# Kernel tuning notes

Hardware: AMD Instinct MI355X
Metric: run time of the kernel (lower is better)

## Reference

```python
import jax, jax.numpy as jnp
import numpy as np

# ----- module constants (from init_kwargs) -----
N = 1024          # Np = [N, N]
NZ = 16           # number of slices (O.shape[3])
NA = 0.65         # objective NA
WL = 0.5          # wavelength (um)
PS = 6.5          # camera pixel size (um)
MAG = 20.0        # magnification
PS_EFF = PS / MAG
DZ = 10.0 * PS / MAG                 # slice spacing (code overwrites wl/na**2)
KAPPA = 2.0 * np.pi * DZ / WL        # imag part of self.k
K = np.complex64(1j * KAPPA)         # self.k as a complex scalar


def _grids():
    c = (np.arange(N) - N // 2) * PS_EFF
    xx, yy = np.meshgrid(c, c)                       # spatial grids
    f = (np.arange(N) - N // 2) / (PS_EFF * N)
    uxx, uyy = np.meshgrid(f, f)                     # frequency grids
    return xx, yy, uxx, uyy

_XX, _YY, _UXX, _UYY = _grids()
_URR = _UXX ** 2 + _UYY ** 2
_PC = (_URR < (NA / WL) ** 2).astype(np.float64)     # centered pupil


def _fresnel(dz):
    # genFrensel: band-limited angular-spectrum kernel, stored in fft order
    kz = np.sqrt(np.maximum(_PC * ((1.0 / WL) ** 2 - _URR), 0.0))
    kern = _PC * np.exp(1j * 2.0 * np.pi * dz * kz)
    return jnp.asarray(np.fft.fftshift(kern).astype(np.complex64))

PUPIL = jnp.asarray(np.fft.fftshift(_PC).astype(np.complex64))   # fft order
PROPKERN = _fresnel(DZ)
PROPKERN_FOCUS = _fresnel(-DZ * (NZ - 1) / 2.0)
XX = jnp.asarray(_XX, jnp.float32)
YY = jnp.asarray(_YY, jnp.float32)


def _prop(u, kern):
    # torch.fft / torch.ifft pair == unnormalized fft2 / normalized ifft2
    return jnp.fft.ifft2(jnp.fft.fft2(u) * kern)


def _plane_wave(na_illum):
    dfx = 1.0 / (PS_EFF * N)
    tilt = jnp.round((na_illum / WL) / dfx) * dfx    # snap tilt to freq grid
    phase = 2.0 * np.pi * (tilt[0] * XX + tilt[1] * YY)
    return jnp.exp(1j * phase)                        # complex64


def _ms_grad(O, intensity, na_illum):
    """Faithful translation of Multislice.grad. O: [N,N,NZ] complex64."""
    T = jnp.exp(K * O)                                # per-slice transmittance
    u = _plane_wave(na_illum)
    # forward multislice propagation
    for zz in range(NZ):
        u = T[..., zz] * u
        if zz < NZ - 1:
            u = _prop(u, PROPKERN)
    # refocus to stack center, apply pupil
    u_ref = _prop(u, PROPKERN_FOCUS)
    u_pup = _prop(u_ref, PUPIL)
    # amplitude-replacement residual
    abs_field = jnp.abs(u_pup)
    comp = jnp.sqrt(intensity) * u_pup / abs_field
    residual = u_pup - comp
    # back-propagate residual
    u_bp = _prop(residual, jnp.conj(PUPIL))
    u_bp = _prop(u_bp, jnp.conj(PROPKERN_FOCUS))
    # reverse slice loop accumulating per-slice gradient
    grads = [None] * NZ
    for zz in range(NZ - 1, -1, -1):
        grads[zz] = u_bp * jnp.conj(u) * jnp.conj(T[..., zz]) * np.conj(K)
        if zz > 0:
            u_bp = _prop(u_bp * jnp.conj(T[..., zz]), jnp.conj(PROPKERN))
            u = _prop(u, jnp.conj(PROPKERN))
            u = u / T[..., zz - 1]
    return jnp.stack(grads, axis=-1)                  # [N,N,NZ] complex


def setup_inputs() -> dict:
    key = jax.random.key(0)
    k1, k2, k3 = jax.random.split(key, 3)
    # small-valued object so exp(i*KAPPA*O) stays bounded (KAPPA ~ 40.8)
    x = jax.random.normal(k1, (N, N, 2, NZ), jnp.float32) * 0.01
    meas = jax.random.uniform(k2, (N, N), jnp.float32) + 0.1
    na_illum = jax.random.uniform(k3, (2,), jnp.float32) * 0.2
    alpha = jnp.full((1,), 0.01, jnp.float32)
    return {"x": x, "meas": meas, "na_illum": na_illum, "alpha": alpha}


def reference(x, meas, na_illum, alpha):
    # forward: x + step(x) = x - alpha * grad(x, meas, na_illum)
    O = x[..., 0, :] + 1j * x[..., 1, :]              # [N,N,NZ] complex64
    g = _ms_grad(O, meas, na_illum)
    out = O - alpha[0] * g
    return jnp.stack((out.real, out.imag), axis=2)    # back to [N,N,2,NZ]
```

## Files before the change

### kernel.cpp

```cpp
#include <hip/hip_runtime.h>
#include <math.h>


#define NN (1024*1024)
#define KAPPA 40.840704496667314f
#define TWO_PI_F 6.2831853071795865f
#define DFX_D 0.0030048076923076925
#define RRCUT 187177
#define F(i) ((i) + ((i)>>4))

#define JT 0
#define JT_WP 1
#define JN 2
#define JRESID 3

__device__ __forceinline__ float2 cmulf(float2 a, float2 b){
    return make_float2(a.x*b.x - a.y*b.y, a.x*b.y + a.y*b.x);
}
__device__ __forceinline__ float2 cmulcj(float2 a, float2 b){
    return make_float2(a.x*b.x + a.y*b.y, a.y*b.x - a.x*b.y);
}
__device__ __forceinline__ float2 f2add(float2 a, float2 b){ return make_float2(a.x+b.x, a.y+b.y); }
__device__ __forceinline__ float2 f2sub(float2 a, float2 b){ return make_float2(a.x-b.x, a.y-b.y); }

__device__ __forceinline__ void fill_tw(float2* tw, int tid){
    #pragma unroll
    for (int k = tid; k < 512; k += 256){
        float s, c; sincosf(-(float)k * (TWO_PI_F/1024.0f), &s, &c);
        tw[k] = make_float2(c, s);
    }
}

__device__ __forceinline__ void dif_ph1(float2 r[8], const float2* tw, int lane){
    float2 a, d;
    #pragma unroll
    for (int k=0;k<4;++k){
        a=r[k]; d=f2sub(r[k],r[k+4]);
        r[k]=f2add(a,r[k+4]);
        r[k+4]=cmulf(d, tw[lane+128*k]);
    }
    float2 w20 = tw[lane<<1], w21 = tw[(lane+128)<<1];
    a=r[0]; d=f2sub(r[0],r[2]); r[0]=f2add(a,r[2]); r[2]=cmulf(d,w20);
    a=r[1]; d=f2sub(r[1],r[3]); r[1]=f2add(a,r[3]); r[3]=cmulf(d,w21);
    a=r[4]; d=f2sub(r[4],r[6]); r[4]=f2add(a,r[6]); r[6]=cmulf(d,w20);
    a=r[5]; d=f2sub(r[5],r[7]); r[5]=f2add(a,r[7]); r[7]=cmulf(d,w21);
    float2 w3 = tw[lane<<2];
    a=r[0]; d=f2sub(r[0],r[1]); r[0]=f2add(a,r[1]); r[1]=cmulf(d,w3);
    a=r[2]; d=f2sub(r[2],r[3]); r[2]=f2add(a,r[3]); r[3]=cmulf(d,w3);
    a=r[4]; d=f2sub(r[4],r[5]); r[4]=f2add(a,r[5]); r[5]=cmulf(d,w3);
    a=r[6]; d=f2sub(r[6],r[7]); r[6]=f2add(a,r[7]); r[7]=cmulf(d,w3);
}
__device__ __forceinline__ void dit_ph1(float2 r[8], const float2* tw, int lane){
    float2 a, b;
    float2 w3 = tw[lane<<2];
    a=r[0]; b=cmulcj(r[1],w3); r[0]=f2add(a,b); r[1]=f2sub(a,b);
    a=r[2]; b=cmulcj(r[3],w3); r[2]=f2add(a,b); r[3]=f2sub(a,b);
    a=r[4]; b=cmulcj(r[5],w3); r[4]=f2add(a,b); r[5]=f2sub(a,b);
    a=r[6]; b=cmulcj(r[7],w3); r[6]=f2add(a,b); r[7]=f2sub(a,b);
    float2 w20 = tw[lane<<1], w21 = tw[(lane+128)<<1];
    a=r[0]; b=cmulcj(r[2],w20); r[0]=f2add(a,b); r[2]=f2sub(a,b);
    a=r[1]; b=cmulcj(r[3],w21); r[1]=f2add(a,b); r[3]=f2sub(a,b);
    a=r[4]; b=cmulcj(r[6],w20); r[4]=f2add(a,b); r[6]=f2sub(a,b);
    a=r[5]; b=cmulcj(r[7],w21); r[5]=f2add(a,b); r[7]=f2sub(a,b);
    #pragma unroll
    for (int k=0;k<4;++k){
        a=r[k]; b=cmulcj(r[k+4], tw[lane+128*k]);
        r[k]=f2add(a,b); r[k+4]=f2sub(a,b);
    }
}
__device__ __forceinline__ void dif_ph2(float2 r[8], const float2* tw, int m0){
    float2 a, d;
    #pragma unroll
    for (int k=0;k<4;++k){
        a=r[k]; d=f2sub(r[k],r[k+4]);
        r[k]=f2add(a,r[k+4]);
        r[k+4]=cmulf(d, tw[(m0+16*k)<<3]);
    }
    float2 w40 = tw[m0<<4], w41 = tw[(m0+16)<<4];
    a=r[0]; d=f2sub(r[0],r[2]); r[0]=f2add(a,r[2]); r[2]=cmulf(d,w40);
    a=r[1]; d=f2sub(r[1],r[3]); r[1]=f2add(a,r[3]); r[3]=cmulf(d,w41);
    a=r[4]; d=f2sub(r[4],r[6]); r[4]=f2add(a,r[6]); r[6]=cmulf(d,w40);
    a=r[5]; d=f2sub(r[5],r[7]); r[5]=f2add(a,r[7]); r[7]=cmulf(d,w41);
    float2 w5 = tw[m0<<5];
    a=r[0]; d=f2sub(r[0],r[1]); r[0]=f2add(a,r[1]); r[1]=cmulf(d,w5);
    a=r[2]; d=f2sub(r[2],r[3]); r[2]=f2add(a,r[3]); r[3]=cmulf(d,w5);
    a=r[4]; d=f2sub(r[4],r[5]); r[4]=f2add(a,r[5]); r[5]=cmulf(d,w5);
    a=r[6]; d=f2sub(r[6],r[7]); r[6]=f2add(a,r[7]); r[7]=cmulf(d,w5);
}
__device__ __forceinline__ void dit_ph2(float2 r[8], const float2* tw, int m0){
    float2 a, b;
    float2 w5 = tw[m0<<5];
    a=r[0]; b=cmulcj(r[1],w5); r[0]=f2add(a,b); r[1]=f2sub(a,b);
    a=r[2]; b=cmulcj(r[3],w5); r[2]=f2add(a,b); r[3]=f2sub(a,b);
    a=r[4]; b=cmulcj(r[5],w5); r[4]=f2add(a,b); r[5]=f2sub(a,b);
    a=r[6]; b=cmulcj(r[7],w5); r[6]=f2add(a,b); r[7]=f2sub(a,b);
    float2 w40 = tw[m0<<4], w41 = tw[(m0+16)<<4];
    a=r[0]; b=cmulcj(r[2],w40); r[0]=f2add(a,b); r[2]=f2sub(a,b);
    a=r[1]; b=cmulcj(r[3],w41); r[1]=f2add(a,b); r[3]=f2sub(a,b);
    a=r[4]; b=cmulcj(r[6],w40); r[4]=f2add(a,b); r[6]=f2sub(a,b);
    a=r[5]; b=cmulcj(r[7],w41); r[5]=f2add(a,b); r[7]=f2sub(a,b);
    #pragma unroll
    for (int k=0;k<4;++k){
        a=r[k]; b=cmulcj(r[k+4], tw[(m0+16*k)<<3]);
        r[k]=f2add(a,b); r[k+4]=f2sub(a,b);
    }
}
__device__ __forceinline__ void dif_reg(float2 r[8]){
    const float C = 0.70710678118654752f;
    float2 a,d;
    a=r[0]; d=f2sub(r[0],r[4]); r[0]=f2add(a,r[4]); r[4]=d;
    a=r[1]; d=f2sub(r[1],r[5]); r[1]=f2add(a,r[5]); r[5]=make_float2(C*(d.x+d.y), C*(d.y-d.x));
    a=r[2]; d=f2sub(r[2],r[6]); r[2]=f2add(a,r[6]); r[6]=make_float2(d.y, -d.x);
    a=r[3]; d=f2sub(r[3],r[7]); r[3]=f2add(a,r[7]); r[7]=make_float2(C*(d.y-d.x), -C*(d.x+d.y));
    a=r[0]; r[0]=f2add(a,r[2]); r[2]=f2sub(a,r[2]);
    a=r[1]; d=f2sub(r[1],r[3]); r[1]=f2add(a,r[3]); r[3]=make_float2(d.y,-d.x);
    a=r[4]; r[4]=f2add(a,r[6]); r[6]=f2sub(a,r[6]);
    a=r[5]; d=f2sub(r[5],r[7]); r[5]=f2add(a,r[7]); r[7]=make_float2(d.y,-d.x);
    a=r[0]; r[0]=f2add(a,r[1]); r[1]=f2sub(a,r[1]);
    a=r[2]; r[2]=f2add(a,r[3]); r[3]=f2sub(a,r[3]);
    a=r[4]; r[4]=f2add(a,r[5]); r[5]=f2sub(a,r[5]);
    a=r[6]; r[6]=f2add(a,r[7]); r[7]=f2sub(a,r[7]);
}
__device__ __forceinline__ void dit_reg(float2 r[8]){
    const float C = 0.70710678118654752f;
    float2 a,b,t;
    a=r[0]; r[0]=f2add(a,r[1]); r[1]=f2sub(a,r[1]);
    a=r[2]; r[2]=f2add(a,r[3]); r[3]=f2sub(a,r[3]);
    a=r[4]; r[4]=f2add(a,r[5]); r[5]=f2sub(a,r[5]);
    a=r[6]; r[6]=f2add(a,r[7]); r[7]=f2sub(a,r[7]);
    a=r[0]; r[0]=f2add(a,r[2]); r[2]=f2sub(a,r[2]);
    a=r[1]; t=r[3]; b=make_float2(-t.y, t.x); r[1]=f2add(a,b); r[3]=f2sub(a,b);
    a=r[4]; r[4]=f2add(a,r[6]); r[6]=f2sub(a,r[6]);
    a=r[5]; t=r[7]; b=make_float2(-t.y, t.x); r[5]=f2add(a,b); r[7]=f2sub(a,b);
    a=r[0]; r[0]=f2add(a,r[4]); r[4]=f2sub(a,r[4]);
    a=r[1]; t=r[5]; b=make_float2(C*(t.x-t.y), C*(t.x+t.y)); r[1]=f2add(a,b); r[5]=f2sub(a,b);
    a=r[2]; t=r[6]; b=make_float2(-t.y, t.x); r[2]=f2add(a,b); r[6]=f2sub(a,b);
    a=r[3]; t=r[7]; b=make_float2(-C*(t.x+t.y), C*(t.x-t.y)); r[3]=f2add(a,b); r[7]=f2sub(a,b);
}

__device__ __forceinline__ void st128l(float2* L, int ro, int lane, const float2 r[8]){
    #pragma unroll
    for (int k=0;k<8;++k) L[F(ro + lane + 128*k)] = r[k];
}
__device__ __forceinline__ void ld128l(const float2* L, int ro, int lane, float2 r[8]){
    #pragma unroll
    for (int k=0;k<8;++k) r[k] = L[F(ro + lane + 128*k)];
}
__device__ __forceinline__ void st16l(float2* L, int ro, int lane, const float2 r[8]){
    int b = lane>>4, m0 = lane&15, q = ro + 128*b + m0;
    #pragma unroll
    for (int k=0;k<8;++k) L[F(q + 16*k)] = r[k];
}
__device__ __forceinline__ void ld16l(const float2* L, int ro, int lane, float2 r[8]){
    int b = lane>>4, m0 = lane&15, q = ro + 128*b + m0;
    #pragma unroll
    for (int k=0;k<8;++k) r[k] = L[F(q + 16*k)];
}
__device__ __forceinline__ void st8l(float2* L, int ro, int lane, const float2 r[8]){
    int q = ro + 8*lane;
    #pragma unroll
    for (int i=0;i<8;++i) L[F(q + i)] = r[i];
}
__device__ __forceinline__ void ldfold_dif(const float2* L, int ro, int lane,
                                           const float2* tw, float2 r[8]){
    int rr = lane>>1, sub = lane&1, q = ro + 16*rr;
    #pragma unroll
    for (int i=0;i<8;++i){
        float2 x = L[F(q + i)];
        float2 y = L[F(q + 8 + i)];
        r[i] = sub ? cmulf(f2sub(x,y), tw[i<<6]) : f2add(x,y);
    }
}
__device__ __forceinline__ void ldfold_dit(const float2* L, int ro, int lane,
                                           const float2* tw, float2 r[8]){
    int b = lane>>4, m0 = lane&15, m0s = m0&7;
    float2 w = tw[m0s<<6];
    int q = ro + 128*b + m0s;
    #pragma unroll
    for (int k=0;k<8;++k){
        float2 x = L[F(q + 16*k)];
        float2 y = L[F(q + 16*k + 8)];
        float2 bb = cmulcj(y, w);
        r[k] = (m0 < 8) ? f2add(x,bb) : f2sub(x,bb);
    }
}
__device__ __forceinline__ void load8g(const float2* src, int lane, float2 r[8]){
    const float4* s4 = (const float4*)src + lane*4;
    #pragma unroll
    for (int m=0;m<4;++m){
        float4 v = s4[m];
        r[2*m]   = make_float2(v.x, v.y);
        r[2*m+1] = make_float2(v.z, v.w);
    }
}
__device__ __forceinline__ void twrite2(const float2* L, int tid, float2* dst,
                                        int r0, float s){
    #pragma unroll
    for (int k=0;k<4;++k){
        int c = tid + (k<<8);
        float2 a0 = L[F(c)], a1 = L[F(1024+c)];
        ((float4*)(dst + ((size_t)c<<10) + r0))[0] =
            make_float4(a0.x*s, a0.y*s, a1.x*s, a1.y*s);
    }
}

__global__ void __launch_bounds__(256) k_kern(float2* __restrict__ kp,
                                              float2* __restrict__ kf){
    int idx = blockIdx.x*256 + threadIdx.x;
    int j = idx >> 10, i = idx & 1023;
    int a = __brev((unsigned)i) >> 22;
    int b = __brev((unsigned)j) >> 22;
    int ra = a - (a >= 512 ? 1024 : 0);
    int rb = b - (b >= 512 ? 1024 : 0);
    int rr = ra*ra + rb*rb;
    float2 p = make_float2(0.f,0.f), f = make_float2(0.f,0.f);
    if (rr <= RRCUT){
        double urr = (double)rr * (DFX_D*DFX_D);
        double kz = sqrt(4.0 - urr);
        double s1,c1,s2,c2;
        sincos(6.283185307179586 * 3.25    * kz, &s1, &c1);
        sincos(6.283185307179586 * -24.375 * kz, &s2, &c2);
        p = make_float2((float)c1,(float)s1);
        f = make_float2((float)c2,(float)s2);
    }
    kp[idx] = p; kf[idx] = f;
}

__global__ void __launch_bounds__(256) k_T(const float4* __restrict__ x,
                                           float2* __restrict__ T){
    int idx = blockIdx.x*256 + threadIdx.x;
    int p = idx >> 2;
    int q = idx & 3;
    float4 vr = x[(size_t)p*8 + q];
    float4 vi = x[(size_t)p*8 + 4 + q];
    const float* fr = (const float*)&vr;
    const float* fi = (const float*)&vi;
    #pragma unroll
    for (int j=0;j<4;++j){
        int z = 4*q + j;
        float amp = __expf(-KAPPA*fi[j]);
        float s, c; __sincosf(KAPPA*fr[j], &s, &c);
        T[(size_t)z*NN + p] = make_float2(amp*c, amp*s);
    }
}

__global__ void __launch_bounds__(256) k_head(float2* __restrict__ dst,
                                              const float2* __restrict__ T0,
                                              const float* __restrict__ nail){
    __shared__ float2 A[2176], B[2176], tw[512];
    const int tid = threadIdx.x;
    fill_tw(tw, tid);
    const int row = tid>>7, lane = tid&127, ro = row<<10, m0 = lane&15;
    const int r0 = blockIdx.x*2;
    const size_t gbase = ((size_t)(r0+row))<<10;
    float dfx = (float)DFX_D;
    float t0 = rintf(nail[0]*2.0f/dfx)*dfx;
    float t1 = rintf(nail[1]*2.0f/dfx)*dfx;
    float yv = (float)((r0+row) - 512) * 0.325f;
    float2 r[8];
    #pragma unroll
    for (int k=0;k<8;++k){
        int col = lane + 128*k;
        float2 tv = T0[gbase + col];
        float xv = (float)(col - 512) * 0.325f;
        float s0, c0; sincosf(TWO_PI_F*(t0*xv + t1*yv), &s0, &c0);
        r[k] = cmulf(make_float2(c0,s0), tv);
    }
    __syncthreads();
    dif_ph1(r, tw, lane);
    st128l(A, ro, lane, r); __syncthreads();
    ld16l(A, ro, lane, r); dif_ph2(r, tw, m0);
    st16l(B, ro, lane, r); __syncthreads();
    ldfold_dif(B, ro, lane, tw, r); dif_reg(r);
    st8l(A, ro, lane, r); __syncthreads();
    twrite2(A, tid, dst, r0, 1.0f);
}

__global__ void __launch_bounds__(256) k_pass2(
    const float2* __restrict__ srcA, float2* __restrict__ dstA,
    const float2* __restrict__ srcB, float2* __restrict__ dstB,
    const float2* __restrict__ km, int conj, int pupil)
{
    __shared__ float2 A[2176], B[2176], tw[512];
    const int tid = threadIdx.x;
    fill_tw(tw, tid);
    const int row = tid>>7, lane = tid&127, ro = row<<10, m0 = lane&15;
    int bid = blockIdx.x;
    const float2* src = srcA; float2* dst = dstA;
    if (srcB != nullptr && bid >= 512){ src = srcB; dst = dstB; bid -= 512; }
    const int r0 = bid*2;
    const int jrow = r0 + row;
    const float2* srcR = src + (((size_t)r0)<<10) + ro;
    float2 r[8];
    #pragma unroll
    for (int k=0;k<8;++k) r[k] = srcR[lane + 128*k];
    float4 kv[4];
    if (!pupil){
        const float4* k4 = (const float4*)(km + (((size_t)jrow)<<10)) + lane*4;
        #pragma unroll
        for (int m=0;m<4;++m) kv[m] = k4[m];
    }
    __syncthreads();
    dif_ph1(r, tw, lane);
    st128l(A, ro, lane, r); __syncthreads();
    ld16l(A, ro, lane, r); dif_ph2(r, tw, m0);
    st16l(B, ro, lane, r); __syncthreads();
    ldfold_dif(B, ro, lane, tw, r); dif_reg(r);
    if (pupil){
        int bb = __brev((unsigned)jrow) >> 22;
        int rb = bb - (bb >= 512 ? 1024 : 0);
        int rb2 = rb*rb;
        #pragma unroll
        for (int i=0;i<8;++i){
            int aa = __brev((unsigned)(8*lane+i)) >> 22;
            int ra = aa - (aa >= 512 ? 1024 : 0);
            if (ra*ra + rb2 > RRCUT) r[i] = make_float2(0.f,0.f);
        }
    } else {
        float sg = conj ? -1.0f : 1.0f;
        #pragma unroll
        for (int m=0;m<4;++m){
            r[2*m]   = cmulf(r[2*m],   make_float2(kv[m].x, sg*kv[m].y));
            r[2*m+1] = cmulf(r[2*m+1], make_float2(kv[m].z, sg*kv[m].w));
        }
    }
    dit_reg(r);
    st8l(A, ro, lane, r); __syncthreads();
    ldfold_dit(A, ro, lane, tw, r); dit_ph2(r, tw, m0);
    st16l(B, ro, lane, r); __syncthreads();
    ld128l(B, ro, lane, r); dit_ph1(r, tw, lane);
    st128l(A, ro, lane, r); __syncthreads();
    twrite2(A, tid, dst, r0, 1.0f/1024.0f);
}

__global__ void __launch_bounds__(256) k_junc(
    const float2* __restrict__ src, float2* __restrict__ dst,
    const float2* __restrict__ Tz, float2* __restrict__ wp,
    const float* __restrict__ meas, int mode)
{
    __shared__ float2 A[2176], B[2176], tw[512];
    const int tid = threadIdx.x;
    fill_tw(tw, tid);
    const int row = tid>>7, lane = tid&127, ro = row<<10, m0 = lane&15;
    const int r0 = blockIdx.x*2;
    const size_t gbase = ((size_t)(r0+row))<<10;
    const float S = 1.0f/1024.0f;
    float2 r[8];
    load8g(src + (((size_t)r0)<<10) + ro, lane, r);
    float2 pre[8];
    if (mode == JT || mode == JT_WP){
        #pragma unroll
        for (int k=0;k<8;++k) pre[k] = Tz[gbase + lane + 128*k];
    } else if (mode == JRESID){
        #pragma unroll
        for (int k=0;k<8;++k) pre[k].x = meas[gbase + lane + 128*k];
    }
    dit_reg(r);
    st8l(A, ro, lane, r); __syncthreads();
    ldfold_dit(A, ro, lane, tw, r); dit_ph2(r, tw, m0);
    st16l(B, ro, lane, r); __syncthreads();
    ld128l(B, ro, lane, r); dit_ph1(r, tw, lane);
    #pragma unroll
    for (int k=0;k<8;++k){
        size_t g = gbase + lane + 128*k;
        float2 v = make_float2(S*r[k].x, S*r[k].y);
        if (mode == JT || mode == JT_WP){
            v = cmulf(v, pre[k]);
            if (mode == JT_WP) wp[g] = v;
        } else if (mode == JRESID){
            float m = pre[k].x;
            float aamp = fmaxf(sqrtf(v.x*v.x + v.y*v.y), 1e-30f);
            float f = 1.0f - sqrtf(m)/aamp;
            v.x *= f; v.y *= f;
        }
        r[k] = v;
    }
    dif_ph1(r, tw, lane);
    st128l(A, ro, lane, r); __syncthreads();
    ld16l(A, ro, lane, r); dif_ph2(r, tw, m0);
    st16l(B, ro, lane, r); __syncthreads();
    ldfold_dif(B, ro, lane, tw, r); dif_reg(r);
    st8l(A, ro, lane, r); __syncthreads();
    twrite2(A, tid, dst, r0, 1.0f);
}

__global__ void __launch_bounds__(256) k_rev(
    const float2* __restrict__ srcU, float2* __restrict__ dstU,
    const float2* __restrict__ srcB, float2* __restrict__ dstB,
    float2* __restrict__ Tz, int headU)
{
    __shared__ float2 A[2176], B[2176], tw[512];
    const int tid = threadIdx.x;
    fill_tw(tw, tid);
    const int row = tid>>7, lane = tid&127, ro = row<<10, m0 = lane&15;
    const int r0 = blockIdx.x*2;
    const size_t gbase = ((size_t)(r0+row))<<10;
    const float S = 1.0f/1024.0f;
    float2 u[8], Tg[8], bb[8], r[8];
    if (!headU){
        load8g(srcU + (((size_t)r0)<<10) + ro, lane, u);
    } else {
        const float2* srcR = srcU + (((size_t)r0)<<10) + ro;
        #pragma unroll
        for (int k=0;k<8;++k) u[k] = srcR[lane + 128*k];
    }
    #pragma unroll
    for (int k=0;k<8;++k) Tg[k] = Tz[gbase + lane + 128*k];
    load8g(srcB + (((size_t)r0)<<10) + ro, lane, bb);
    if (!headU){
        dit_reg(u);
        st8l(A, ro, lane, u); __syncthreads();
        ldfold_dit(A, ro, lane, tw, u); dit_ph2(u, tw, m0);
        st16l(B, ro, lane, u); __syncthreads();
        ld128l(B, ro, lane, u); dit_ph1(u, tw, lane);
        #pragma unroll
        for (int k=0;k<8;++k){ u[k].x *= S; u[k].y *= S; }
    } else {
        __syncthreads();
    }
    #pragma unroll
    for (int k=0;k<8;++k){
        if (headU) r[k] = u[k];
        else {
            float inv = 1.0f/(Tg[k].x*Tg[k].x + Tg[k].y*Tg[k].y);
            float2 wc = cmulcj(u[k], Tg[k]);
            r[k] = make_float2(wc.x*inv, wc.y*inv);
        }
    }
    dif_ph1(r, tw, lane);
    st128l(A, ro, lane, r); __syncthreads();
    ld16l(A, ro, lane, r); dif_ph2(r, tw, m0);
    st16l(B, ro, lane, r); __syncthreads();
    ldfold_dif(B, ro, lane, tw, r); dif_reg(r);
    st8l(A, ro, lane, r); __syncthreads();
    twrite2(A, tid, dstU, r0, 1.0f);
    dit_reg(bb);
    st8l(B, ro, lane, bb); __syncthreads();
    ldfold_dit(B, ro, lane, tw, r); dit_ph2(r, tw, m0);
    st16l(A, ro, lane, r); __syncthreads();
    ld128l(A, ro, lane, r); dit_ph1(r, tw, lane);
    #pragma unroll
    for (int k=0;k<8;++k){
        float2 b = make_float2(S*r[k].x, S*r[k].y);
        float2 q = headU ? cmulcj(cmulcj(b, u[k]), Tg[k]) : cmulcj(b, u[k]);
        Tz[gbase + lane + 128*k] = make_float2(KAPPA*q.y, -KAPPA*q.x);
        r[k] = cmulcj(b, Tg[k]);
    }
    dif_ph1(r, tw, lane);
    st128l(B, ro, lane, r); __syncthreads();
    ld16l(B, ro, lane, r); dif_ph2(r, tw, m0);
    st16l(A, ro, lane, r); __syncthreads();
    ldfold_dif(A, ro, lane, tw, r); dif_reg(r);
    st8l(B, ro, lane, r); __syncthreads();
    twrite2(B, tid, dstB, r0, 1.0f);
}

__global__ void __launch_bounds__(256) k_tail(
    const float2* __restrict__ srcU, const float2* __restrict__ srcB,
    float2* __restrict__ G0)
{
    __shared__ float2 A[2176], B[2176], tw[512];
    const int tid = threadIdx.x;
    fill_tw(tw, tid);
    const int row = tid>>7, lane = tid&127, ro = row<<10, m0 = lane&15;
    const int r0 = blockIdx.x*2;
    const size_t gbase = ((size_t)(r0+row))<<10;
    const float S = 1.0f/1024.0f;
    float2 u[8], r[8];
    load8g(srcU + (((size_t)r0)<<10) + ro, lane, u);
    load8g(srcB + (((size_t)r0)<<10) + ro, lane, r);
    dit_reg(u);
    st8l(A, ro, lane, u); __syncthreads();
    ldfold_dit(A, ro, lane, tw, u); dit_ph2(u, tw, m0);
    st16l(B, ro, lane, u); __syncthreads();
    ld128l(B, ro, lane, u); dit_ph1(u, tw, lane);
    dit_reg(r);
    st8l(A, ro, lane, r); __syncthreads();
    ldfold_dit(A, ro, lane, tw, r); dit_ph2(r, tw, m0);
    st16l(B, ro, lane, r); __syncthreads();
    ld128l(B, ro, lane, r); dit_ph1(r, tw, lane);
    #pragma unroll
    for (int k=0;k<8;++k){
        float2 b = make_float2(S*r[k].x, S*r[k].y);
        float2 w = make_float2(S*u[k].x, S*u[k].y);
        float2 q = cmulcj(b, w);
        G0[gbase + lane + 128*k] = make_float2(KAPPA*q.y, -KAPPA*q.x);
    }
}

__global__ void __launch_bounds__(256) k_merge(const float4* __restrict__ x,
                                               const float2* __restrict__ G,
                                               const float* __restrict__ alpha,
                                               float4* __restrict__ out){
    int idx4 = blockIdx.x*256 + threadIdx.x;
    int p  = idx4 >> 3;
    int f  = idx4 & 7;
    int c  = f >> 2;
    int zb = (f & 3) * 4;
    float al = alpha[0];
    float4 xv = x[idx4];
    float gc[4];
    #pragma unroll
    for (int j=0;j<4;++j){
        float2 g = G[(size_t)(zb + j)*NN + p];
        gc[j] = c ? g.y : g.x;
    }
    out[idx4] = make_float4(xv.x - al*gc[0], xv.y - al*gc[1],
                            xv.z - al*gc[2], xv.w - al*gc[3]);
}

extern "C" void kernel_launch(void* const* d_in, const int* in_sizes, int n_in,
                              void* d_out, int out_size, void* d_ws, size_t ws_size,
                              hipStream_t stream)
{
    const float* x     = (const float*)d_in[0];
    const float* meas  = (const float*)d_in[1];
    const float* nail  = (const float*)d_in[2];
    const float* alpha = (const float*)d_in[3];

    if (ws_size < (size_t)23*NN*sizeof(float2)) return;

    float2* W   = (float2*)d_ws;
    float2* T   = W;
    float2* KP  = W + (size_t)16*NN;
    float2* KF  = W + (size_t)17*NN;
    float2* U0  = W + (size_t)18*NN;
    float2* TAB = W + (size_t)19*NN;
    float2* TBB = W + (size_t)20*NN;
    float2* TAU = W + (size_t)21*NN;
    float2* TBU = W + (size_t)22*NN;

    k_kern<<<4096, 256, 0, stream>>>(KP, KF);
    k_T   <<<16384, 256, 0, stream>>>((const float4*)x, T);

    auto P2f = [&](const float2* km, int cj, int pup){
        k_pass2<<<512, 256, 0, stream>>>(TAB, TBB, nullptr, nullptr, km, cj, pup);
    };

    k_head<<<512, 256, 0, stream>>>(TAB, T, nail);
    P2f(KP, 0, 0);
    for (int z = 1; z <= 14; ++z){
        k_junc<<<512, 256, 0, stream>>>(TBB, TAB, T + (size_t)z*NN, nullptr, nullptr, JT);
        P2f(KP, 0, 0);
    }
    k_junc<<<512, 256, 0, stream>>>(TBB, TAB, T + (size_t)15*NN, U0, nullptr, JT_WP);
    P2f(KF, 0, 0);
    k_junc<<<512, 256, 0, stream>>>(TBB, TAB, nullptr, nullptr, nullptr, JN);
    P2f(nullptr, 0, 1);
    k_junc<<<512, 256, 0, stream>>>(TBB, TAB, nullptr, nullptr, meas, JRESID);
    P2f(nullptr, 1, 1);
    k_junc<<<512, 256, 0, stream>>>(TBB, TAB, nullptr, nullptr, nullptr, JN);
    P2f(KF, 1, 0);

    for (int zz = 15; zz >= 1; --zz){
        k_rev<<<512, 256, 0, stream>>>(zz == 15 ? U0 : TBU, TAU, TBB, TAB,
                                       T + (size_t)zz*NN, zz == 15 ? 1 : 0);
        k_pass2<<<1024, 256, 0, stream>>>(TAB, TBB, TAU, TBU, KP, 1, 0);
    }
    k_tail<<<512, 256, 0, stream>>>(TBU, TBB, T);

    k_merge<<<32768, 256, 0, stream>>>((const float4*)x, T, alpha, (float4*)d_out);
}
```

Baseline: 1.461 ms.

## Compute propagation kernels on the fly, fuse pupil into Fresnel passes, vectorize T/merge

Drops the precomputed propagation-kernel tables and evaluates the angular-spectrum phase in double precision inside each FFT pass, which removes the kernel-table reads. Because the Fresnel kernel is already zero outside the pupil, the separate pupil-only passes and their junction launches are folded away, giving four fewer full-image FFT round trips. k_T and k_merge are rewritten so each thread handles two pixels or both real and imaginary halves with wider stores. In exchange every pass now pays for a double-precision sqrt per element, which is costly in ALU time on the hot path.

Measured after the change: 1.421 ms. 2.7% less time.

```diff
diff --git a/kernel.cpp b/kernel.cpp
--- a/kernel.cpp
+++ b/kernel.cpp
@@ -11,7 +11,6 @@
 
 #define JT 0
 #define JT_WP 1
-#define JN 2
 #define JRESID 3
 
 __device__ __forceinline__ float2 cmulf(float2 a, float2 b){
@@ -204,46 +203,6 @@
     }
 }
 
-__global__ void __launch_bounds__(256) k_kern(float2* __restrict__ kp,
-                                              float2* __restrict__ kf){
-    int idx = blockIdx.x*256 + threadIdx.x;
-    int j = idx >> 10, i = idx & 1023;
-    int a = __brev((unsigned)i) >> 22;
-    int b = __brev((unsigned)j) >> 22;
-    int ra = a - (a >= 512 ? 1024 : 0);
-    int rb = b - (b >= 512 ? 1024 : 0);
-    int rr = ra*ra + rb*rb;
-    float2 p = make_float2(0.f,0.f), f = make_float2(0.f,0.f);
-    if (rr <= RRCUT){
-        double urr = (double)rr * (DFX_D*DFX_D);
-        double kz = sqrt(4.0 - urr);
-        double s1,c1,s2,c2;
-        sincos(6.283185307179586 * 3.25    * kz, &s1, &c1);
-        sincos(6.283185307179586 * -24.375 * kz, &s2, &c2);
-        p = make_float2((float)c1,(float)s1);
-        f = make_float2((float)c2,(float)s2);
-    }
-    kp[idx] = p; kf[idx] = f;
-}
-
-__global__ void __launch_bounds__(256) k_T(const float4* __restrict__ x,
-                                           float2* __restrict__ T){
-    int idx = blockIdx.x*256 + threadIdx.x;
-    int p = idx >> 2;
-    int q = idx & 3;
-    float4 vr = x[(size_t)p*8 + q];
-    float4 vi = x[(size_t)p*8 + 4 + q];
-    const float* fr = (const float*)&vr;
-    const float* fi = (const float*)&vi;
-    #pragma unroll
-    for (int j=0;j<4;++j){
-        int z = 4*q + j;
-        float amp = __expf(-KAPPA*fi[j]);
-        float s, c; __sincosf(KAPPA*fr[j], &s, &c);
-        T[(size_t)z*NN + p] = make_float2(amp*c, amp*s);
-    }
-}
-
 __global__ void __launch_bounds__(256) k_head(float2* __restrict__ dst,
                                               const float2* __restrict__ T0,
                                               const float* __restrict__ nail){
@@ -279,7 +238,7 @@
 __global__ void __launch_bounds__(256) k_pass2(
     const float2* __restrict__ srcA, float2* __restrict__ dstA,
     const float2* __restrict__ srcB, float2* __restrict__ dstB,
-    const float2* __restrict__ km, int conj, int pupil)
+    double zscale, float sg)
 {
     __shared__ float2 A[2176], B[2176], tw[512];
     const int tid = threadIdx.x;
@@ -294,19 +253,13 @@
     float2 r[8];
     #pragma unroll
     for (int k=0;k<8;++k) r[k] = srcR[lane + 128*k];
-    float4 kv[4];
-    if (!pupil){
-        const float4* k4 = (const float4*)(km + (((size_t)jrow)<<10)) + lane*4;
-        #pragma unroll
-        for (int m=0;m<4;++m) kv[m] = k4[m];
-    }
     __syncthreads();
     dif_ph1(r, tw, lane);
     st128l(A, ro, lane, r); __syncthreads();
     ld16l(A, ro, lane, r); dif_ph2(r, tw, m0);
     st16l(B, ro, lane, r); __syncthreads();
     ldfold_dif(B, ro, lane, tw, r); dif_reg(r);
-    if (pupil){
+    {
         int bb = __brev((unsigned)jrow) >> 22;
         int rb = bb - (bb >= 512 ? 1024 : 0);
         int rb2 = rb*rb;
@@ -314,14 +267,17 @@
         for (int i=0;i<8;++i){
             int aa = __brev((unsigned)(8*lane+i)) >> 22;
             int ra = aa - (aa >= 512 ? 1024 : 0);
-            if (ra*ra + rb2 > RRCUT) r[i] = make_float2(0.f,0.f);
-        }
-    } else {
-        float sg = conj ? -1.0f : 1.0f;
-        #pragma unroll
-        for (int m=0;m<4;++m){
-            r[2*m]   = cmulf(r[2*m],   make_float2(kv[m].x, sg*kv[m].y));
-            r[2*m+1] = cmulf(r[2*m+1], make_float2(kv[m].z, sg*kv[m].w));
+            int rr = ra*ra + rb2;
+            if (rr <= RRCUT){
+                double urr = (double)rr * (DFX_D*DFX_D);
+                double kz = sqrt(4.0 - urr);
+                double t = zscale * kz;
+                float fp = (float)(t - floor(t));
+                float s, c; sincosf(TWO_PI_F*fp, &s, &c);
+                r[i] = cmulf(r[i], make_float2(c, sg*s));
+            } else {
+                r[i] = make_float2(0.f, 0.f);
+            }
         }
     }
     dit_reg(r);
@@ -488,25 +444,47 @@
     }
 }
 
+__global__ void __launch_bounds__(256) k_T(const float4* __restrict__ x,
+                                           float2* __restrict__ T){
+    int idx = blockIdx.x*256 + threadIdx.x;
+    int pp = idx >> 2;
+    int q  = idx & 3;
+    int p0 = pp*2;
+    float4 vr0 = x[(size_t)p0*8 + q];
+    float4 vi0 = x[(size_t)p0*8 + 4 + q];
+    float4 vr1 = x[(size_t)(p0+1)*8 + q];
+    float4 vi1 = x[(size_t)(p0+1)*8 + 4 + q];
+    const float* fr0 = (const float*)&vr0;
+    const float* fi0 = (const float*)&vi0;
+    const float* fr1 = (const float*)&vr1;
+    const float* fi1 = (const float*)&vi1;
+    #pragma unroll
+    for (int j=0;j<4;++j){
+        int z = 4*q + j;
+        float a0 = __expf(-KAPPA*fi0[j]);
+        float s0, c0; __sincosf(KAPPA*fr0[j], &s0, &c0);
+        float a1 = __expf(-KAPPA*fi1[j]);
+        float s1, c1; __sincosf(KAPPA*fr1[j], &s1, &c1);
+        ((float4*)(T + (size_t)z*NN + p0))[0] = make_float4(a0*c0, a0*s0, a1*c1, a1*s1);
+    }
+}
+
 __global__ void __launch_bounds__(256) k_merge(const float4* __restrict__ x,
                                                const float2* __restrict__ G,
                                                const float* __restrict__ alpha,
                                                float4* __restrict__ out){
-    int idx4 = blockIdx.x*256 + threadIdx.x;
-    int p  = idx4 >> 3;
-    int f  = idx4 & 7;
-    int c  = f >> 2;
-    int zb = (f & 3) * 4;
+    int idx = blockIdx.x*256 + threadIdx.x;
+    int p = idx >> 2, q = idx & 3;
     float al = alpha[0];
-    float4 xv = x[idx4];
-    float gc[4];
-    #pragma unroll
-    for (int j=0;j<4;++j){
-        float2 g = G[(size_t)(zb + j)*NN + p];
-        gc[j] = c ? g.y : g.x;
-    }
-    out[idx4] = make_float4(xv.x - al*gc[0], xv.y - al*gc[1],
-                            xv.z - al*gc[2], xv.w - al*gc[3]);
+    float4 xr = x[(size_t)p*8 + q];
+    float4 xi = x[(size_t)p*8 + 4 + q];
+    float2 g[4];
+    #pragma unroll
+    for (int j=0;j<4;++j) g[j] = G[(size_t)(4*q+j)*NN + p];
+    out[(size_t)p*8 + q]     = make_float4(xr.x - al*g[0].x, xr.y - al*g[1].x,
+                                           xr.z - al*g[2].x, xr.w - al*g[3].x);
+    out[(size_t)p*8 + 4 + q] = make_float4(xi.x - al*g[0].y, xi.y - al*g[1].y,
+                                           xi.z - al*g[2].y, xi.w - al*g[3].y);
 }
 
 extern "C" void kernel_launch(void* const* d_in, const int* in_sizes, int n_in,
@@ -518,46 +496,42 @@
     const float* nail  = (const float*)d_in[2];
     const float* alpha = (const float*)d_in[3];
 
-    if (ws_size < (size_t)23*NN*sizeof(float2)) return;
+    if (ws_size < (size_t)21*NN*sizeof(float2)) return;
 
     float2* W   = (float2*)d_ws;
     float2* T   = W;
-    float2* KP  = W + (size_t)16*NN;
-    float2* KF  = W + (size_t)17*NN;
-    float2* U0  = W + (size_t)18*NN;
-    float2* TAB = W + (size_t)19*NN;
-    float2* TBB = W + (size_t)20*NN;
-    float2* TAU = W + (size_t)21*NN;
-    float2* TBU = W + (size_t)22*NN;
-
-    k_kern<<<4096, 256, 0, stream>>>(KP, KF);
-    k_T   <<<16384, 256, 0, stream>>>((const float4*)x, T);
-
-    auto P2f = [&](const float2* km, int cj, int pup){
-        k_pass2<<<512, 256, 0, stream>>>(TAB, TBB, nullptr, nullptr, km, cj, pup);
+    float2* U0  = W + (size_t)16*NN;
+    float2* TAB = W + (size_t)17*NN;
+    float2* TBB = W + (size_t)18*NN;
+    float2* TAU = W + (size_t)19*NN;
+    float2* TBU = W + (size_t)20*NN;
+
+    const double ZP = 3.25;
+    const double ZF = -24.375;
+
+    k_T <<<8192, 256, 0, stream>>>((const float4*)x, T);
+
+    auto P2f = [&](double zs, float sg){
+        k_pass2<<<512, 256, 0, stream>>>(TAB, TBB, nullptr, nullptr, zs, sg);
     };
 
     k_head<<<512, 256, 0, stream>>>(TAB, T, nail);
-    P2f(KP, 0, 0);
+    P2f(ZP, 1.0f);
     for (int z = 1; z <= 14; ++z){
         k_junc<<<512, 256, 0, stream>>>(TBB, TAB, T + (size_t)z*NN, nullptr, nullptr, JT);
-        P2f(KP, 0, 0);
+        P2f(ZP, 1.0f);
     }
     k_junc<<<512, 256, 0, stream>>>(TBB, TAB, T + (size_t)15*NN, U0, nullptr, JT_WP);
-    P2f(KF, 0, 0);
-    k_junc<<<512, 256, 0, stream>>>(TBB, TAB, nullptr, nullptr, nullptr, JN);
-    P2f(nullptr, 0, 1);
+    P2f(ZF, 1.0f);
     k_junc<<<512, 256, 0, stream>>>(TBB, TAB, nullptr, nullptr, meas, JRESID);
-    P2f(nullptr, 1, 1);
-    k_junc<<<512, 256, 0, stream>>>(TBB, TAB, nullptr, nullptr, nullptr, JN);
-    P2f(KF, 1, 0);
+    P2f(ZF, -1.0f);
 
     for (int zz = 15; zz >= 1; --zz){
         k_rev<<<512, 256, 0, stream>>>(zz == 15 ? U0 : TBU, TAU, TBB, TAB,
                                        T + (size_t)zz*NN, zz == 15 ? 1 : 0);
-        k_pass2<<<1024, 256, 0, stream>>>(TAB, TBB, TAU, TBU, KP, 1, 0);
+        k_pass2<<<1024, 256, 0, stream>>>(TAB, TBB, TAU, TBU, ZP, -1.0f);
     }
     k_tail<<<512, 256, 0, stream>>>(TBU, TBB, T);
 
-    k_merge<<<32768, 256, 0, stream>>>((const float4*)x, T, alpha, (float4*)d_out);
-}
+    k_merge<<<16384, 256, 0, stream>>>((const float4*)x, T, alpha, (float4*)d_out);
+}
```
